# Performance work log

Measured on AMD Instinct MI355X. Metric: run time of the kernel, lower is better.

The kernel has to match this reference:

```python
import jax, jax.numpy as jnp
import numpy as np

EMBED_DIM = 768
NUM_HEADS = 12
PROJ_DIM = EMBED_DIM // NUM_HEADS  # 64
M_FEATURES = 128
EPS = 1e-6


def _orthogonal_projection(key, m, d):
    # Faithful to create_projection_matrix(scaling=0): stacked transposed Q-factors
    # of iid gaussian blocks, rescaled by chi-distributed row norms.
    nb_full_blocks = m // d
    keys = jax.random.split(key, nb_full_blocks + 2)
    blocks = []
    for i in range(nb_full_blocks):
        q, _ = jnp.linalg.qr(jax.random.normal(keys[i], (d, d)))
        blocks.append(q.T)
    rem = m - nb_full_blocks * d
    if rem > 0:
        q, _ = jnp.linalg.qr(jax.random.normal(keys[nb_full_blocks], (d, d)))
        blocks.append(q.T[:rem])
    final = jnp.vstack(blocks)
    multiplier = jnp.linalg.norm(jax.random.normal(keys[-1], (m, d)), axis=1)
    return multiplier[:, None] * final


def setup_inputs() -> dict:
    key = jax.random.key(0)
    ks = jax.random.split(key, 8)
    B, L, E = 4, 4096, EMBED_DIM
    s = 1.0 / np.sqrt(E)
    inp = {
        "x": jax.random.normal(ks[0], (B, L, E), jnp.float32),
        "Wq": jax.random.normal(ks[1], (E, E), jnp.float32) * s,
        "bq": jnp.zeros((E,), jnp.float32),
        "Wk": jax.random.normal(ks[2], (E, E), jnp.float32) * s,
        "bk": jnp.zeros((E,), jnp.float32),
        "Wv": jax.random.normal(ks[3], (E, E), jnp.float32) * s,
        "bv": jnp.zeros((E,), jnp.float32),
        "Wo": jax.random.normal(ks[4], (E, E), jnp.float32) * s,
        "bo": jnp.zeros((E,), jnp.float32),
        "proj": _orthogonal_projection(ks[5], M_FEATURES, PROJ_DIM),
    }
    return inp


def _softmax_kernel(data, projection_matrix):
    # data: [B, L, H, D]; projection_matrix: [M, D]
    data_normalizer = 1.0 / jnp.sqrt(jnp.sqrt(jnp.float32(PROJ_DIM)))
    data = data_normalizer * data
    ratio = 1.0 / jnp.sqrt(jnp.float32(projection_matrix.shape[0]))
    data_dash = jnp.einsum("blhd,md->blhm", data, projection_matrix)
    diag_data = jnp.sum(jnp.square(data), axis=-1, keepdims=True) / 2.0  # [B,L,H,1]
    stab = jnp.max(data_dash, axis=-1, keepdims=True)
    return ratio * (jnp.exp(data_dash - diag_data - stab) + EPS)


def reference(x, Wq, bq, Wk, bk, Wv, bv, Wo, bo, proj):
    B, L, E = x.shape
    H, D = NUM_HEADS, PROJ_DIM

    def split_heads(t):
        return t.reshape(B, L, H, D)

    q = split_heads(x @ Wq + bq)
    k = split_heads(x @ Wk + bk)
    v = split_heads(x @ Wv + bv)

    q_prime = _softmax_kernel(q, proj)  # [B,L,H,M]
    k_prime = _softmax_kernel(k, proj)  # [B,L,H,M]

    # Linear-attention numerator/denominator (O(L) in sequence length).
    kvs = jnp.einsum("blhm,blhd->bhmd", k_prime, v)          # [B,H,M,D]
    num = jnp.einsum("blhm,bhmd->blhd", q_prime, kvs)        # [B,L,H,D]
    ks_sum = jnp.sum(k_prime, axis=1)                         # [B,H,M]
    den = jnp.einsum("blhm,bhm->blh", q_prime, ks_sum)        # [B,L,H]
    attention = num / den[..., None]                          # [B,L,H,D]

    # Faithful to source: transpose to [B,H,L,D] then reshape to [B,-1,E].
    concat = jnp.transpose(attention, (0, 2, 1, 3)).reshape(B, -1, E)
    return concat @ Wo + bo
```

## Files before the change

### kernel.cpp

```cpp
#include <hip/hip_runtime.h>

typedef _Float16 f16;
typedef __attribute__((ext_vector_type(8))) _Float16 half8;
typedef __attribute__((ext_vector_type(4))) _Float16 half4;
typedef __attribute__((ext_vector_type(4))) float f32x4;

#define DEVINL static __device__ __forceinline__

constexpr float NORMALIZER = 0.35355339059327373f;
constexpr float RATIO      = 0.08838834764831845f;
constexpr float FEPS       = 1e-6f;

constexpr size_t OFF_WQKVT = 0;
constexpr size_t OFF_WOT   = OFF_WQKVT + (size_t)2304*768*2;
constexpr size_t OFF_PROJF = OFF_WOT   + (size_t)768*768*2;
constexpr size_t OFF_KS    = OFF_PROJF + (size_t)128*64*2;
constexpr size_t OFF_KSP   = OFF_KS    + (size_t)48*128*4;
constexpr size_t OFF_KVST  = OFF_KSP   + (size_t)48*64*128*4;
constexpr size_t OFF_KVSP  = OFF_KVST  + (size_t)48*64*128*2;
constexpr size_t OFF_X16   = OFF_KVSP  + (size_t)16*48*128*64*4;
constexpr size_t OFF_ATT   = OFF_X16;
constexpr size_t OFF_Q16   = OFF_X16 + (size_t)16384*768*2;
constexpr size_t OFF_K16   = OFF_Q16 + (size_t)16384*768*2;
constexpr size_t OFF_VT    = OFF_K16 + (size_t)16384*768*2;
constexpr size_t OFF_KPT   = OFF_VT  + (size_t)16384*768*2;

DEVINL void gload_lds16(const f16* g, f16* lds) {
  __builtin_amdgcn_global_load_lds(
      (const __attribute__((address_space(1))) void*)g,
      (__attribute__((address_space(3))) void*)lds, 16, 0, 0);
}

#define VMCNT0    asm volatile("s_waitcnt vmcnt(0)" ::: "memory")
#define BAR       __builtin_amdgcn_s_barrier()

DEVINL void gemm256c(const f16* __restrict__ Ag, const f16* __restrict__ Bg,
                     f16* smem, f32x4 (&acc)[8][3], int w, int lane)
{
  constexpr int NT = 24;
  const int wm = w >> 2, wn = w & 3;
  const int c = lane & 15, g16 = lane >> 4;
  const int tid = threadIdx.x;

#pragma unroll
  for (int i = 0; i < 8; ++i)
#pragma unroll
    for (int j = 0; j < 3; ++j)
      acc[i][j] = f32x4{0.f, 0.f, 0.f, 0.f};

  auto SA = [&](int tt, f16* buf) {
#pragma unroll
    for (int u = 0; u < 2; ++u) {
      const int id = u * 512 + tid;
      const int r = id >> 2, sg = id & 3;
      const int seg = sg ^ ((r >> 1) & 3);
      gload_lds16(Ag + (size_t)r * 768 + tt * 32 + seg * 8, buf + (u * 512 + w * 64) * 8);
    }
  };
  auto SB = [&](int tt, f16* buf) {
    {
      const int r = tid >> 2, sg = tid & 3;
      const int seg = sg ^ ((r >> 1) & 3);
      gload_lds16(Bg + (size_t)r * 768 + tt * 32 + seg * 8, buf + 8192 + w * 64 * 8);
    }
    if (w < 4) {
      const int id = 512 + tid;
      const int r = id >> 2, sg = id & 3;
      const int seg = sg ^ ((r >> 1) & 3);
      gload_lds16(Bg + (size_t)r * 768 + tt * 32 + seg * 8, buf + 8192 + (512 + w * 64) * 8);
    }
  };
  auto RDA = [&](const f16* buf, int mh, half8 (&av)[4]) {
#pragma unroll
    for (int i = 0; i < 4; ++i) {
      const int r = wm * 128 + mh * 64 + i * 16 + c;
      av[i] = *(const half8*)(buf + r * 32 + ((g16 ^ ((r >> 1) & 3)) << 3));
    }
  };
  auto RDB = [&](const f16* buf, half8 (&bv)[3]) {
#pragma unroll
    for (int j = 0; j < 3; ++j) {
      const int r = wn * 48 + j * 16 + c;
      bv[j] = *(const half8*)(buf + 8192 + r * 32 + ((g16 ^ ((r >> 1) & 3)) << 3));
    }
  };

  SA(0, smem); SB(0, smem);
  VMCNT0;
  BAR;

#pragma unroll 1
  for (int t = 0; t < NT; ++t) {
    f16* bufR = smem + (t & 1) * 14336;
    f16* bufW = smem + ((t & 1) ^ 1) * 14336;
    const bool st = (t + 1) < NT;
    half8 av[4], bv[3];

    RDA(bufR, 0, av); RDB(bufR, bv);
    if (st) SA(t + 1, bufW);
    __builtin_amdgcn_s_setprio(1);
#pragma unroll
    for (int i = 0; i < 4; ++i)
#pragma unroll
      for (int j = 0; j < 3; ++j)
        acc[i][j] = __builtin_amdgcn_mfma_f32_16x16x32_f16(av[i], bv[j], acc[i][j], 0, 0, 0);
    __builtin_amdgcn_s_setprio(0);
    RDA(bufR, 1, av);
    if (st) SB(t + 1, bufW);
    __builtin_amdgcn_s_setprio(1);
#pragma unroll
    for (int i = 0; i < 4; ++i)
#pragma unroll
      for (int j = 0; j < 3; ++j)
        acc[4 + i][j] = __builtin_amdgcn_mfma_f32_16x16x32_f16(av[i], bv[j], acc[4 + i][j], 0, 0, 0);
    __builtin_amdgcn_s_setprio(0);
    VMCNT0;
    BAR;
  }
}

__global__ __launch_bounds__(512, 2) void k_gemm_qkv8(const f16* __restrict__ X16, const f16* __restrict__ WT,
    const float* __restrict__ bq, const float* __restrict__ bk, const float* __restrict__ bv,
    f16* __restrict__ Qo, f16* __restrict__ Ko, f16* __restrict__ VT)
{
  __shared__ f16 smem[28672];
  f32x4 acc[8][3];
  const int lin = blockIdx.x;
  const int xcd = lin & 7, chunk = lin >> 3;
  const int bx = xcd * 8 + chunk / 12;
  const int by = chunk % 12;
  const int brow0 = bx * 256;
  const int t = threadIdx.x, w = t >> 6, lane = t & 63;
  gemm256c(X16 + (size_t)brow0 * 768, WT + (size_t)by * 192 * 768, smem, acc, w, lane);

  const int wm = w >> 2, wn = w & 3;
  const int c = lane & 15, g16 = lane >> 4;
  const int which = by >> 2;
  const int colhdr = (by & 3) * 192;
  const float* bias = which == 0 ? bq : (which == 1 ? bk : bv);
  float bb[3];
#pragma unroll
  for (int j = 0; j < 3; ++j) bb[j] = bias[colhdr + wn * 48 + j * 16 + c];

  f16* ep = smem;
  if (which < 2) {
    f16* QK = which == 0 ? Qo : Ko;
#pragma unroll 1
    for (int p = 0; p < 2; ++p) {
      __syncthreads();
      if (wm == p) {
#pragma unroll
        for (int ii = 0; ii < 8; ++ii)
#pragma unroll
          for (int j = 0; j < 3; ++j)
#pragma unroll
            for (int r = 0; r < 4; ++r)
              ep[((ii >> 2) * 64 + (ii & 3) * 16 + g16 * 4 + r) * 200 + wn * 48 + j * 16 + c]
                  = (f16)(acc[ii][j][r] + bb[j]);
      }
      __syncthreads();
      const int row = t >> 2, sg = (t & 3) * 48;
      f16* dst = QK + (size_t)(brow0 + p * 128 + row) * 768 + colhdr + sg;
      const f16* sp = ep + row * 200 + sg;
#pragma unroll
      for (int u = 0; u < 6; ++u) *(half8*)(dst + u * 8) = *(const half8*)(sp + u * 8);
    }
  } else {
    const int bIdx = brow0 >> 12;
#pragma unroll 1
    for (int p = 0; p < 2; ++p) {
      __syncthreads();
      if (wm == p) {
#pragma unroll
        for (int ii = 0; ii < 8; ++ii)
#pragma unroll
          for (int j = 0; j < 3; ++j)
#pragma unroll
            for (int r = 0; r < 4; ++r)
              ep[(wn * 48 + j * 16 + c) * 136 + (ii >> 2) * 64 + (ii & 3) * 16 + g16 * 4 + r]
                  = (f16)(acc[ii][j][r] + bb[j]);
      }
      __syncthreads();
      if (t < 384) {
        const int cl = t >> 1, sg = (t & 1) * 64;
        const int vcol = colhdr + cl;
        const int h = vcol >> 6, d = vcol & 63;
        f16* dst = VT + ((size_t)(bIdx * 12 + h) * 64 + d) * 4096 + (brow0 & 4095) + p * 128 + sg;
        const f16* sp = ep + cl * 136 + sg;
#pragma unroll
        for (int u = 0; u < 8; ++u) *(half8*)(dst + u * 8) = *(const half8*)(sp + u * 8);
      }
    }
  }
}

__global__ __launch_bounds__(512, 2) void k_gemm_out8(const f16* __restrict__ ATT, const f16* __restrict__ WOT,
    const float* __restrict__ bo, float* __restrict__ out)
{
  __shared__ f16 smem[28672];
  f32x4 acc[8][3];
  const int lin = blockIdx.x;
  const int xcd = lin & 7, chunk = lin >> 3;
  const int bx = xcd * 8 + (chunk >> 2);
  const int by = chunk & 3;
  const int brow0 = bx * 256;
  const int t = threadIdx.x, w = t >> 6, lane = t & 63;
  gemm256c(ATT + (size_t)brow0 * 768, WOT + (size_t)by * 192 * 768, smem, acc, w, lane);

  const int wm = w >> 2, wn = w & 3;
  const int c = lane & 15, g16 = lane >> 4;
  float bb[3];
#pragma unroll
  for (int j = 0; j < 3; ++j) bb[j] = bo[by * 192 + wn * 48 + j * 16 + c];
#pragma unroll
  for (int ii = 0; ii < 8; ++ii) {
    const int row0 = brow0 + wm * 128 + (ii >> 2) * 64 + (ii & 3) * 16 + g16 * 4;
#pragma unroll
    for (int j = 0; j < 3; ++j) {
      const int col = by * 192 + wn * 48 + j * 16 + c;
#pragma unroll
      for (int r = 0; r < 4; ++r)
        out[(size_t)(row0 + r) * 768 + col] = acc[ii][j][r] + bb[j];
    }
  }
}

template<int BN>
DEVINL void gemm_tile(const f16* A, int lda, const f16* Bt, int ldb, int K,
                      f16* As, f16* Bs, f32x4 (&acc)[4][BN/32])
{
  constexpr int NF = BN/32;
  const int t = threadIdx.x;
  const int w = t >> 6, lane = t & 63;
  const int g = lane >> 4, c = lane & 15;
  const int wr = w >> 1, wc = w & 1;
  const int srow = lane >> 2;
  const int sseg = (lane & 3) * 8;

#pragma unroll
  for (int i = 0; i < 4; ++i)
#pragma unroll
    for (int j = 0; j < NF; ++j)
      acc[i][j] = f32x4{0.f, 0.f, 0.f, 0.f};

  for (int k0 = 0; k0 < K; k0 += 32) {
#pragma unroll
    for (int r = 0; r < 2; ++r) {
      const int rowblk = (w + 4*r) * 16;
      gload_lds16(A + (size_t)(rowblk + srow) * lda + k0 + sseg, As + rowblk*32);
    }
#pragma unroll
    for (int r = 0; r < BN/64; ++r) {
      const int rowblk = (w + 4*r) * 16;
      gload_lds16(Bt + (size_t)(rowblk + srow) * ldb + k0 + sseg, Bs + rowblk*32);
    }
    __syncthreads();
    half8 av[4], bv[NF];
#pragma unroll
    for (int i = 0; i < 4; ++i)
      av[i] = *(const half8*)(As + (wr*64 + i*16 + c)*32 + g*8);
#pragma unroll
    for (int j = 0; j < NF; ++j)
      bv[j] = *(const half8*)(Bs + (wc*(BN/2) + j*16 + c)*32 + g*8);
#pragma unroll
    for (int i = 0; i < 4; ++i)
#pragma unroll
      for (int j = 0; j < NF; ++j)
        acc[i][j] = __builtin_amdgcn_mfma_f32_16x16x32_f16(av[i], bv[j], acc[i][j], 0, 0, 0);
    __syncthreads();
  }
}

__global__ __launch_bounds__(256) void k_cast_x(const float* __restrict__ X, f16* __restrict__ X16)
{
  const size_t i = ((size_t)blockIdx.x*256 + threadIdx.x) * 4;
  const float4 v = *(const float4*)(X + i);
  half4 h;
  h[0] = (f16)v.x; h[1] = (f16)v.y; h[2] = (f16)v.z; h[3] = (f16)v.w;
  *(half4*)(X16 + i) = h;
}

__global__ __launch_bounds__(256) void k_transpose_w4(const float* __restrict__ Wq, const float* __restrict__ Wk,
    const float* __restrict__ Wv, const float* __restrict__ Wo, f16* __restrict__ WQKVT, f16* __restrict__ WOT)
{
  __shared__ float ls[64][65];
  const int t = threadIdx.x;
  const int k0 = blockIdx.x*64, n0 = blockIdx.y*64, z = blockIdx.z;
  const float* W = z == 0 ? Wq : (z == 1 ? Wk : (z == 2 ? Wv : Wo));
  f16* Wt = z < 3 ? (WQKVT + (size_t)z*768*768) : WOT;
#pragma unroll
  for (int it = 0; it < 4; ++it) {
    const int r = it*16 + (t >> 4);
    const int cs = (t & 15) * 4;
    const float4 v = *(const float4*)(W + (size_t)(k0 + r)*768 + n0 + cs);
    ls[r][cs+0] = v.x; ls[r][cs+1] = v.y; ls[r][cs+2] = v.z; ls[r][cs+3] = v.w;
  }
  __syncthreads();
  const int n = t >> 2;
  const int seg = (t & 3) * 16;
  half8 ov[2];
#pragma unroll
  for (int i = 0; i < 16; ++i) ov[i>>3][i&7] = (f16)ls[seg + i][n];
  f16* dst = Wt + (size_t)(n0 + n)*768 + k0 + seg;
  *(half8*)dst = ov[0];
  *(half8*)(dst + 8) = ov[1];
}

__global__ __launch_bounds__(256) void k_cast_proj(const float* __restrict__ P, f16* __restrict__ PF)
{
  const int i = blockIdx.x*256 + threadIdx.x;
  PF[i] = (f16)(NORMALIZER * P[i]);
}

DEVINL void feat_common(const f16* base, const f16* PROJF,
                        f16* qs, f16* ps, float* dd, float* diag_s)
{
  const int t = threadIdx.x, w = t >> 6, lane = t & 63;
#pragma unroll
  for (int it = 0; it < 2; ++it) {
    const int rowblk = it*32 + w*8;
    gload_lds16(base + (size_t)(rowblk + (lane>>3))*768 + (lane&7)*8, qs + rowblk*64);
  }
#pragma unroll
  for (int it = 0; it < 4; ++it) {
    const int rowblk = it*32 + w*8;
    gload_lds16(PROJF + (size_t)(rowblk + (lane>>3))*64 + (lane&7)*8, ps + rowblk*64);
  }
  __syncthreads();
  if (t < 64) {
    float s = 0.f;
    for (int d = 0; d < 64; ++d) { const float qv = (float)qs[t*64 + d]; s += qv*qv; }
    diag_s[t] = 0.0625f * s;
  }
  const int g = lane >> 4, c = lane & 15;
  const int wr = w >> 1, wc = w & 1;
  f32x4 facc[2][4];
#pragma unroll
  for (int i = 0; i < 2; ++i)
#pragma unroll
    for (int j = 0; j < 4; ++j) facc[i][j] = f32x4{0.f,0.f,0.f,0.f};
#pragma unroll
  for (int kk = 0; kk < 2; ++kk) {
    half8 av[2], bv[4];
#pragma unroll
    for (int i = 0; i < 2; ++i) av[i] = *(const half8*)(qs + (wr*32 + i*16 + c)*64 + kk*32 + g*8);
#pragma unroll
    for (int j = 0; j < 4; ++j) bv[j] = *(const half8*)(ps + (wc*64 + j*16 + c)*64 + kk*32 + g*8);
#pragma unroll
    for (int i = 0; i < 2; ++i)
#pragma unroll
      for (int j = 0; j < 4; ++j)
        facc[i][j] = __builtin_amdgcn_mfma_f32_16x16x32_f16(av[i], bv[j], facc[i][j], 0, 0, 0);
  }
#pragma unroll
  for (int i = 0; i < 2; ++i)
#pragma unroll
    for (int j = 0; j < 4; ++j)
#pragma unroll
      for (int r = 0; r < 4; ++r)
        dd[(wr*32 + i*16 + g*4 + r)*129 + wc*64 + j*16 + c] = facc[i][j][r];
  __syncthreads();
}

__global__ __launch_bounds__(256) void k_kfeat(const f16* __restrict__ Kin, const f16* __restrict__ PROJF,
    f16* __restrict__ KPT, float* __restrict__ KSP)
{
  __shared__ f16 qs[64*64];
  __shared__ f16 ps[128*64];
  __shared__ float dd[64*129];
  __shared__ float diag_s[64];
  const int t = threadIdx.x;
  const int lb = blockIdx.x, bh = blockIdx.y;
  const int b = bh / 12, h = bh - b*12;
  feat_common(Kin + ((size_t)(b*4096 + lb*64))*768 + h*64, PROJF, qs, ps, dd, diag_s);
  const int l = t >> 2, s = t & 3;
  float v[32];
#pragma unroll
  for (int j = 0; j < 32; ++j) v[j] = dd[l*129 + s*32 + j];
  float mx = v[0];
#pragma unroll
  for (int j = 1; j < 32; ++j) mx = fmaxf(mx, v[j]);
  mx = fmaxf(mx, __shfl_xor(mx, 1));
  mx = fmaxf(mx, __shfl_xor(mx, 2));
  const float off = diag_s[l] + mx;
#pragma unroll
  for (int j = 0; j < 32; ++j) dd[l*129 + s*32 + j] = RATIO * (__expf(v[j] - off) + FEPS);
  __syncthreads();
  if (t < 128) {
    float sm = 0.f;
    for (int l2 = 0; l2 < 64; ++l2) sm += dd[l2*129 + t];
    KSP[((size_t)bh*64 + lb)*128 + t] = sm;
  }
  const int m = t >> 1, hf = t & 1;
  half8 ov[4];
#pragma unroll
  for (int i2 = 0; i2 < 32; ++i2) ov[i2>>3][i2&7] = (f16)dd[(hf*32 + i2)*129 + m];
  f16* dst = KPT + ((size_t)bh*128 + m)*4096 + lb*64 + hf*32;
#pragma unroll
  for (int q8 = 0; q8 < 4; ++q8) *(half8*)(dst + q8*8) = ov[q8];
}

__global__ __launch_bounds__(256) void k_kvs(const f16* __restrict__ KPT, const f16* __restrict__ VT,
    float* __restrict__ KVSP)
{
  __shared__ f16 As[128*32], Bs[64*32];
  f32x4 acc[4][2];
  const int chunk = blockIdx.x, bh = blockIdx.y;
  gemm_tile<64>(KPT + (size_t)bh*128*4096 + chunk*256, 4096,
                VT  + (size_t)bh*64*4096  + chunk*256, 4096, 256, As, Bs, acc);
  const int t = threadIdx.x, w = t>>6, lane = t&63, g = lane>>4, c = lane&15;
  const int wr = w>>1, wc = w&1;
  float* dst = KVSP + (size_t)(chunk*48 + bh)*128*64;
#pragma unroll
  for (int i = 0; i < 4; ++i) {
    const int row0 = wr*64 + i*16 + g*4;
#pragma unroll
    for (int j = 0; j < 2; ++j) {
      const int col = wc*32 + j*16 + c;
#pragma unroll
      for (int r = 0; r < 4; ++r) dst[(size_t)(row0 + r)*64 + col] = acc[i][j][r];
    }
  }
}

__global__ __launch_bounds__(256) void k_reduce(const float* __restrict__ KVSP, const float* __restrict__ KSP,
    f16* __restrict__ KVST, float* __restrict__ KS)
{
  const int i = blockIdx.x*256 + threadIdx.x;
  if (i < 48*128*64) {
    const int bh = i >> 13, md = i & 8191, m = md >> 6, d = md & 63;
    float s = 0.f;
#pragma unroll
    for (int c = 0; c < 16; ++c) s += KVSP[((size_t)(c*48 + bh)*128 + m)*64 + d];
    KVST[((size_t)bh*64 + d)*128 + m] = (f16)s;
  }
  if (i < 48*128) {
    const int bh = i >> 7, m = i & 127;
    float s = 0.f;
#pragma unroll 8
    for (int lb = 0; lb < 64; ++lb) s += KSP[((size_t)bh*64 + lb)*128 + m];
    KS[i] = s;
  }
}

__global__ __launch_bounds__(256) void k_qfn(const f16* __restrict__ Q, const f16* __restrict__ PROJF,
    const float* __restrict__ KS, const f16* __restrict__ KVST, f16* __restrict__ ATT)
{
  __shared__ f16 qs[64*64];
  __shared__ f16 ps[128*64];
  __shared__ float dd[64*129];
  __shared__ float diag_s[64];
  __shared__ float den_s[64];
  __shared__ f16 qp[64*128];
  __shared__ float ks_s[128];
  const int t = threadIdx.x;
  const int lb = blockIdx.x, bh = blockIdx.y;
  const int b = bh / 12, h = bh - b*12;
  if (t < 128) ks_s[t] = KS[bh*128 + t];
  feat_common(Q + ((size_t)(b*4096 + lb*64))*768 + h*64, PROJF, qs, ps, dd, diag_s);

  const int w = t >> 6, lane = t & 63, g16 = lane >> 4, c = lane & 15;
  const int wr = w >> 1, wc = w & 1;
  half8 bv2[2][4];
#pragma unroll
  for (int j = 0; j < 2; ++j) {
    const int d = wc*32 + j*16 + c;
#pragma unroll
    for (int kk = 0; kk < 4; ++kk)
      bv2[j][kk] = *(const half8*)(KVST + (size_t)bh*8192 + d*128 + kk*32 + g16*8);
  }

  const int l = t >> 2, s = t & 3;
  float v[32];
#pragma unroll
  for (int j = 0; j < 32; ++j) v[j] = dd[l*129 + s*32 + j];
  float mx = v[0];
#pragma unroll
  for (int j = 1; j < 32; ++j) mx = fmaxf(mx, v[j]);
  mx = fmaxf(mx, __shfl_xor(mx, 1));
  mx = fmaxf(mx, __shfl_xor(mx, 2));
  const float off = diag_s[l] + mx;
  half8 ov[4];
  float dp = 0.f;
#pragma unroll
  for (int j = 0; j < 32; ++j) {
    const float e = RATIO * (__expf(v[j] - off) + FEPS);
    ov[j>>3][j&7] = (f16)e;
    dp += e * ks_s[s*32 + j];
  }
  dp += __shfl_xor(dp, 1);
  dp += __shfl_xor(dp, 2);
  if (s == 0) den_s[l] = dp;
#pragma unroll
  for (int k = 0; k < 4; ++k)
    *(half8*)(qp + l*128 + (((4*s + k) ^ (l & 7)) << 3)) = ov[k];
  __syncthreads();

  f32x4 acc2[2][2];
#pragma unroll
  for (int i = 0; i < 2; ++i)
#pragma unroll
    for (int j = 0; j < 2; ++j) acc2[i][j] = f32x4{0.f,0.f,0.f,0.f};
#pragma unroll
  for (int kk = 0; kk < 4; ++kk) {
    half8 av2[2];
#pragma unroll
    for (int i = 0; i < 2; ++i) {
      const int l2 = wr*32 + i*16 + c;
      av2[i] = *(const half8*)(qp + l2*128 + (((kk*4 + g16) ^ (l2 & 7)) << 3));
    }
#pragma unroll
    for (int i = 0; i < 2; ++i)
#pragma unroll
      for (int j = 0; j < 2; ++j)
        acc2[i][j] = __builtin_amdgcn_mfma_f32_16x16x32_f16(av2[i], bv2[j][kk], acc2[i][j], 0, 0, 0);
  }

  f16* ep = ps;
#pragma unroll
  for (int i = 0; i < 2; ++i)
#pragma unroll
    for (int j = 0; j < 2; ++j)
#pragma unroll
      for (int r = 0; r < 4; ++r) {
        const int l3 = wr*32 + i*16 + g16*4 + r;
        ep[l3*72 + wc*32 + j*16 + c] = (f16)(acc2[i][j][r] / den_s[l3]);
      }
  __syncthreads();
  const int row = t >> 2, sg = (t & 3) * 16;
  f16* dst = ATT + ((size_t)bh*4096 + lb*64 + row)*64 + sg;
  const f16* sp = ep + row*72 + sg;
  *(half8*)dst = *(const half8*)sp;
  *(half8*)(dst + 8) = *(const half8*)(sp + 8);
}

extern "C" void kernel_launch(void* const* d_in, const int* in_sizes, int n_in,
                              void* d_out, int out_size, void* d_ws, size_t ws_size,
                              hipStream_t stream)
{
  const float* x    = (const float*)d_in[0];
  const float* Wq   = (const float*)d_in[1];
  const float* bq   = (const float*)d_in[2];
  const float* Wk   = (const float*)d_in[3];
  const float* bk   = (const float*)d_in[4];
  const float* Wv   = (const float*)d_in[5];
  const float* bv   = (const float*)d_in[6];
  const float* Wo   = (const float*)d_in[7];
  const float* bo   = (const float*)d_in[8];
  const float* proj = (const float*)d_in[9];
  float* out = (float*)d_out;
  char* ws = (char*)d_ws;

  f16*   WQKVT = (f16*)(ws + OFF_WQKVT);
  f16*   WOT   = (f16*)(ws + OFF_WOT);
  f16*   PROJF = (f16*)(ws + OFF_PROJF);
  float* KS    = (float*)(ws + OFF_KS);
  float* KSP   = (float*)(ws + OFF_KSP);
  f16*   KVST  = (f16*)(ws + OFF_KVST);
  float* KVSP  = (float*)(ws + OFF_KVSP);
  f16*   X16   = (f16*)(ws + OFF_X16);
  f16*   ATT   = (f16*)(ws + OFF_ATT);
  f16*   Q16   = (f16*)(ws + OFF_Q16);
  f16*   K16   = (f16*)(ws + OFF_K16);
  f16*   VT    = (f16*)(ws + OFF_VT);
  f16*   KPT   = (f16*)(ws + OFF_KPT);

  k_cast_x<<<12288, 256, 0, stream>>>(x, X16);
  k_transpose_w4<<<dim3(12,12,4), 256, 0, stream>>>(Wq, Wk, Wv, Wo, WQKVT, WOT);
  k_cast_proj<<<32, 256, 0, stream>>>(proj, PROJF);

  k_gemm_qkv8<<<768, 512, 0, stream>>>(X16, WQKVT, bq, bk, bv, Q16, K16, VT);
  k_kfeat<<<dim3(64,48), 256, 0, stream>>>(K16, PROJF, KPT, KSP);
  k_kvs<<<dim3(16,48), 256, 0, stream>>>(KPT, VT, KVSP);
  k_reduce<<<1536, 256, 0, stream>>>(KVSP, KSP, KVST, KS);
  k_qfn<<<dim3(64,48), 256, 0, stream>>>(Q16, PROJF, KS, KVST, ATT);
  k_gemm_out8<<<256, 512, 0, stream>>>(ATT, WOT, bo, out);
}
```

Baseline: 257.2 us.

## Fuse split-K reduction into kvs kernel via last-block atomic counter

```diff
diff --git a/kernel.cpp b/kernel.cpp
--- a/kernel.cpp
+++ b/kernel.cpp
@@ -17,8 +17,9 @@
 constexpr size_t OFF_KS    = OFF_PROJF + (size_t)128*64*2;
 constexpr size_t OFF_KSP   = OFF_KS    + (size_t)48*128*4;
 constexpr size_t OFF_KVST  = OFF_KSP   + (size_t)48*64*128*4;
-constexpr size_t OFF_KVSP  = OFF_KVST  + (size_t)48*64*128*2;
-constexpr size_t OFF_X16   = OFF_KVSP  + (size_t)16*48*128*64*4;
+constexpr size_t OFF_CNT   = OFF_KVST  + (size_t)48*64*128*2;
+constexpr size_t OFF_KVSP  = OFF_CNT   + 4096;
+constexpr size_t OFF_X16   = OFF_KVSP  + (size_t)8*48*128*64*4;
 constexpr size_t OFF_ATT   = OFF_X16;
 constexpr size_t OFF_Q16   = OFF_X16 + (size_t)16384*768*2;
 constexpr size_t OFF_K16   = OFF_Q16 + (size_t)16384*768*2;
@@ -271,13 +272,18 @@
   }
 }
 
-__global__ __launch_bounds__(256) void k_cast_x(const float* __restrict__ X, f16* __restrict__ X16)
+__global__ __launch_bounds__(256) void k_cast_x(const float* __restrict__ X, f16* __restrict__ X16,
+    const float* __restrict__ P, f16* __restrict__ PF, int* __restrict__ CNT)
 {
   const size_t i = ((size_t)blockIdx.x*256 + threadIdx.x) * 4;
   const float4 v = *(const float4*)(X + i);
   half4 h;
   h[0] = (f16)v.x; h[1] = (f16)v.y; h[2] = (f16)v.z; h[3] = (f16)v.w;
   *(half4*)(X16 + i) = h;
+  if (blockIdx.x == 0) {
+    for (int i2 = threadIdx.x; i2 < 8192; i2 += 256) PF[i2] = (f16)(NORMALIZER * P[i2]);
+    if (threadIdx.x < 48) CNT[threadIdx.x] = 0;
+  }
 }
 
 __global__ __launch_bounds__(256) void k_transpose_w4(const float* __restrict__ Wq, const float* __restrict__ Wk,
@@ -306,12 +312,6 @@
   *(half8*)(dst + 8) = ov[1];
 }
 
-__global__ __launch_bounds__(256) void k_cast_proj(const float* __restrict__ P, f16* __restrict__ PF)
-{
-  const int i = blockIdx.x*256 + threadIdx.x;
-  PF[i] = (f16)(NORMALIZER * P[i]);
-}
-
 DEVINL void feat_common(const f16* base, const f16* PROJF,
                         f16* qs, f16* ps, float* dd, float* diag_s)
 {
@@ -327,10 +327,19 @@
     gload_lds16(PROJF + (size_t)(rowblk + (lane>>3))*64 + (lane&7)*8, ps + rowblk*64);
   }
   __syncthreads();
-  if (t < 64) {
+  {
+    const int row = t >> 2, q = t & 3;
+    const f16* kr = qs + row*64 + q*16;
+    half8 v0 = *(const half8*)(kr);
+    half8 v1 = *(const half8*)(kr + 8);
     float s = 0.f;
-    for (int d = 0; d < 64; ++d) { const float qv = (float)qs[t*64 + d]; s += qv*qv; }
-    diag_s[t] = 0.0625f * s;
+#pragma unroll
+    for (int d2 = 0; d2 < 8; ++d2) { float a = (float)v0[d2]; s += a*a; }
+#pragma unroll
+    for (int d2 = 0; d2 < 8; ++d2) { float a = (float)v1[d2]; s += a*a; }
+    s += __shfl_xor(s, 1);
+    s += __shfl_xor(s, 2);
+    if (q == 0) diag_s[row] = 0.0625f * s;
   }
   const int g = lane >> 4, c = lane & 15;
   const int wr = w >> 1, wc = w & 1;
@@ -386,10 +395,13 @@
 #pragma unroll
   for (int j = 0; j < 32; ++j) dd[l*129 + s*32 + j] = RATIO * (__expf(v[j] - off) + FEPS);
   __syncthreads();
-  if (t < 128) {
+  {
+    const int m = t >> 1, hf = t & 1;
     float sm = 0.f;
-    for (int l2 = 0; l2 < 64; ++l2) sm += dd[l2*129 + t];
-    KSP[((size_t)bh*64 + lb)*128 + t] = sm;
+#pragma unroll 8
+    for (int l2 = hf*32; l2 < hf*32 + 32; ++l2) sm += dd[l2*129 + m];
+    sm += __shfl_xor(sm, 1);
+    if (hf == 0) KSP[((size_t)bh*64 + lb)*128 + m] = sm;
   }
   const int m = t >> 1, hf = t & 1;
   half8 ov[4];
@@ -401,13 +413,14 @@
 }
 
 __global__ __launch_bounds__(256) void k_kvs(const f16* __restrict__ KPT, const f16* __restrict__ VT,
-    float* __restrict__ KVSP)
+    float* __restrict__ KVSP, const float* __restrict__ KSP, f16* __restrict__ KVST,
+    float* __restrict__ KS, int* __restrict__ CNT)
 {
   __shared__ f16 As[128*32], Bs[64*32];
   f32x4 acc[4][2];
   const int chunk = blockIdx.x, bh = blockIdx.y;
-  gemm_tile<64>(KPT + (size_t)bh*128*4096 + chunk*256, 4096,
-                VT  + (size_t)bh*64*4096  + chunk*256, 4096, 256, As, Bs, acc);
+  gemm_tile<64>(KPT + (size_t)bh*128*4096 + chunk*512, 4096,
+                VT  + (size_t)bh*64*4096  + chunk*512, 4096, 512, As, Bs, acc);
   const int t = threadIdx.x, w = t>>6, lane = t&63, g = lane>>4, c = lane&15;
   const int wr = w>>1, wc = w&1;
   float* dst = KVSP + (size_t)(chunk*48 + bh)*128*64;
@@ -421,25 +434,27 @@
       for (int r = 0; r < 4; ++r) dst[(size_t)(row0 + r)*64 + col] = acc[i][j][r];
     }
   }
-}
-
-__global__ __launch_bounds__(256) void k_reduce(const float* __restrict__ KVSP, const float* __restrict__ KSP,
-    f16* __restrict__ KVST, float* __restrict__ KS)
-{
-  const int i = blockIdx.x*256 + threadIdx.x;
-  if (i < 48*128*64) {
-    const int bh = i >> 13, md = i & 8191, m = md >> 6, d = md & 63;
-    float s = 0.f;
-#pragma unroll
-    for (int c = 0; c < 16; ++c) s += KVSP[((size_t)(c*48 + bh)*128 + m)*64 + d];
-    KVST[((size_t)bh*64 + d)*128 + m] = (f16)s;
-  }
-  if (i < 48*128) {
-    const int bh = i >> 7, m = i & 127;
-    float s = 0.f;
+
+  __threadfence();
+  __syncthreads();
+  __shared__ int lastFlag;
+  if (t == 0) lastFlag = (atomicAdd(&CNT[bh], 1) == 7);
+  __syncthreads();
+  if (lastFlag) {
+    __threadfence();
+    for (int i = t; i < 128*64; i += 256) {
+      const int m = i >> 6, d = i & 63;
+      float s = 0.f;
+#pragma unroll
+      for (int c2 = 0; c2 < 8; ++c2) s += KVSP[((size_t)(c2*48 + bh)*128 + m)*64 + d];
+      KVST[((size_t)bh*64 + d)*128 + m] = (f16)s;
+    }
+    for (int i = t; i < 128; i += 256) {
+      float s = 0.f;
 #pragma unroll 8
-    for (int lb = 0; lb < 64; ++lb) s += KSP[((size_t)bh*64 + lb)*128 + m];
-    KS[i] = s;
+      for (int lb = 0; lb < 64; ++lb) s += KSP[((size_t)bh*64 + lb)*128 + i];
+      KS[bh*128 + i] = s;
+    }
   }
 }
 
@@ -557,6 +572,7 @@
   float* KS    = (float*)(ws + OFF_KS);
   float* KSP   = (float*)(ws + OFF_KSP);
   f16*   KVST  = (f16*)(ws + OFF_KVST);
+  int*   CNT   = (int*)(ws + OFF_CNT);
   float* KVSP  = (float*)(ws + OFF_KVSP);
   f16*   X16   = (f16*)(ws + OFF_X16);
   f16*   ATT   = (f16*)(ws + OFF_ATT);
@@ -565,14 +581,12 @@
   f16*   VT    = (f16*)(ws + OFF_VT);
   f16*   KPT   = (f16*)(ws + OFF_KPT);
 
-  k_cast_x<<<12288, 256, 0, stream>>>(x, X16);
+  k_cast_x<<<12288, 256, 0, stream>>>(x, X16, proj, PROJF, CNT);
   k_transpose_w4<<<dim3(12,12,4), 256, 0, stream>>>(Wq, Wk, Wv, Wo, WQKVT, WOT);
-  k_cast_proj<<<32, 256, 0, stream>>>(proj, PROJF);
 
   k_gemm_qkv8<<<768, 512, 0, stream>>>(X16, WQKVT, bq, bk, bv, Q16, K16, VT);
   k_kfeat<<<dim3(64,48), 256, 0, stream>>>(K16, PROJF, KPT, KSP);
-  k_kvs<<<dim3(16,48), 256, 0, stream>>>(KPT, VT, KVSP);
-  k_reduce<<<1536, 256, 0, stream>>>(KVSP, KSP, KVST, KS);
+  k_kvs<<<dim3(8,48), 256, 0, stream>>>(KPT, VT, KVSP, KSP, KVST, KS, CNT);
   k_qfn<<<dim3(64,48), 256, 0, stream>>>(Q16, PROJF, KS, KVST, ATT);
   k_gemm_out8<<<256, 512, 0, stream>>>(ATT, WOT, bo, out);
 }
```

New measurement: 342.2 us. 33.1% more time.
